# Performance work log

Measured on AMD Instinct MI355X. Metric: run time of the kernel, lower is better.

The kernel has to match this reference:

```python
import jax, jax.numpy as jnp
import numpy as np

LN_EPS = 1e-5
BN_EPS = 1e-5
N_TARGETS = 7


def setup_inputs() -> dict:
    key = jax.random.key(0)
    ks = jax.random.split(key, 12)
    B, N, W, Fin = 64, 40, 256, 64
    H, D = 4, 32
    C = H * D  # gat_out = 128
    L, K = 4, 3  # tcn layers / kernel
    FC = 128
    x = jax.random.normal(ks[0], (B, N, W, Fin), dtype=jnp.float32)
    adj = (jax.random.uniform(ks[1], (N, N)) < 0.3).astype(jnp.float32)
    adj = jnp.maximum(adj, jnp.eye(N, dtype=jnp.float32))  # self-loops
    s = 0.05
    return {
        "x": x,
        "adj": adj,
        "gat_w": jax.random.normal(ks[2], (C, Fin), dtype=jnp.float32) * s,
        "a_src": jax.random.normal(ks[3], (H, D), dtype=jnp.float32) * s,
        "a_dst": jax.random.normal(ks[4], (H, D), dtype=jnp.float32) * s,
        "ln_g": jnp.ones((C,), jnp.float32),
        "ln_b": jnp.zeros((C,), jnp.float32),
        "c1w": jax.random.normal(ks[5], (L, C, C, K), dtype=jnp.float32) * s,
        "c1b": jnp.zeros((L, C), jnp.float32),
        "c2w": jax.random.normal(ks[6], (L, C, C, K), dtype=jnp.float32) * s,
        "c2b": jnp.zeros((L, C), jnp.float32),
        "bn1s": jnp.ones((L, C), jnp.float32),
        "bn1b": jnp.zeros((L, C), jnp.float32),
        "bn1m": jnp.zeros((L, C), jnp.float32),
        "bn1v": jnp.ones((L, C), jnp.float32),
        "bn2s": jnp.ones((L, C), jnp.float32),
        "bn2b": jnp.zeros((L, C), jnp.float32),
        "bn2m": jnp.zeros((L, C), jnp.float32),
        "bn2v": jnp.ones((L, C), jnp.float32),
        "f1w": jax.random.normal(ks[7], (FC, C), dtype=jnp.float32) * s,
        "f1b": jnp.zeros((FC,), jnp.float32),
        "f2w": jax.random.normal(ks[8], (1, FC), dtype=jnp.float32) * s,
        "f2b": jnp.zeros((1,), jnp.float32),
    }


def reference(x, adj, gat_w, a_src, a_dst, ln_g, ln_b,
              c1w, c1b, c2w, c2b,
              bn1s, bn1b, bn1m, bn1v, bn2s, bn2b, bn2m, bn2v,
              f1w, f1b, f2w, f2b):
    B, N, W, Fin = x.shape
    H, D = a_src.shape
    C = H * D
    # --- GAT, vectorized over all W timesteps at once (same math as the per-t loop) ---
    h = jnp.einsum('bnwf,of->bnwo', x, gat_w).reshape(B, N, W, H, D)
    e_src = jnp.einsum('bnwhd,hd->bnwh', h, a_src)  # (B,N,W,H)
    e_dst = jnp.einsum('bnwhd,hd->bnwh', h, a_dst)
    # scores[b,i,w,h,j] = leaky_relu(e_src[b,i] + e_dst[b,j])
    scores = e_src[:, :, :, :, None] + jnp.transpose(e_dst, (0, 2, 3, 1))[:, None]  # (B,N,W,H,N)
    scores = jax.nn.leaky_relu(scores, 0.2)
    mask = adj[None, :, None, None, :] != 0
    scores = jnp.where(mask, scores, -1e9)
    attn = jax.nn.softmax(scores, axis=-1)  # softmax over destination j
    gat = jnp.einsum('bnwhj,bjwhd->bnwhd', attn, h).reshape(B, N, W, C)
    # --- LayerNorm over feature dim ---
    mu = gat.mean(-1, keepdims=True)
    var = gat.var(-1, keepdims=True)
    g = (gat - mu) / jnp.sqrt(var + LN_EPS) * ln_g + ln_b
    # --- TCN over per-node temporal sequences: (B*N, C, W) ---
    seq = jnp.transpose(g.reshape(B * N, W, C), (0, 2, 1))
    K = c1w.shape[-1]

    def bn(z, s, b, m, v):
        return (z - m[None, :, None]) / jnp.sqrt(v[None, :, None] + BN_EPS) * s[None, :, None] + b[None, :, None]

    def cconv(z, w, b, dil):
        pad = (K - 1) * dil  # causal left-padding
        y = jax.lax.conv_general_dilated(z, w, window_strides=(1,), padding=[(pad, 0)],
                                         rhs_dilation=(dil,), dimension_numbers=('NCH', 'OIH', 'NCH'))
        return y + b[None, :, None]

    cur = seq
    for i in range(c1w.shape[0]):  # fixed small number of TCN blocks
        dil = 2 ** i
        o = jax.nn.gelu(bn(cconv(cur, c1w[i], c1b[i], dil), bn1s[i], bn1b[i], bn1m[i], bn1v[i]), approximate=False)
        o = jax.nn.gelu(bn(cconv(o, c2w[i], c2b[i], dil), bn2s[i], bn2b[i], bn2m[i], bn2v[i]), approximate=False)
        cur = jax.nn.gelu(o + cur, approximate=False)  # residual is Identity (in_ch == out_ch)
    h_last = cur[:, :, -1].reshape(B, N, C)
    t = h_last[:, :N_TARGETS, :]  # target_indices = range(7)
    z = jax.nn.gelu(jnp.einsum('bnc,hc->bnh', t, f1w) + f1b, approximate=False)
    logits = (jnp.einsum('bnh,oh->bno', z, f2w) + f2b)[..., 0]  # (B, 7)
    return logits
```

## Files before the change

### kernel.cpp

```cpp
#include <hip/hip_runtime.h>
#include <hip/hip_bf16.h>
#include <math.h>

#define Bb   64
#define Nn   40
#define Ww   256
#define FIN  64
#define Hh   4
#define Dd   32
#define Cc   128
#define NT   7
#define FC   128
#define WT   61
#define W0   195
#define PSTRIDE 520
#define HS2  132

#define GTAUS 2
#define NTG   31
#define XPAN  768
#define GROWS 80

#define SEQHI_OFF  0u
#define SEQ_BYTES  (448u * WT * Cc * 2u)
#define SEQLO_OFF  (SEQHI_OFF + SEQ_BYTES)
#define WBH_OFF    (SEQLO_OFF + SEQ_BYTES)
#define WB_BYTES   (8u * 4u * 24u * 64u * 8u * 2u)
#define WBL_OFF    (WBH_OFF + WB_BYTES)
#define PSB_OFF    (WBL_OFF + WB_BYTES)
#define PSS_OFF    (PSB_OFF + 4096u)
#define PSH_OFF    (PSS_OFF + 4096u)
#define WGH_OFF    (PSH_OFF + 4096u)
#define WGL_OFF    (WGH_OFF + 16384u)
#define WPHASE_US  49152u

typedef __attribute__((ext_vector_type(8)))  short short8;
typedef __attribute__((ext_vector_type(16))) float f32x16;

__device__ __forceinline__ float gelu_exact(float v) {
    const float z = v * 0.70710678118654752440f;
    const float a = fabsf(z);
    const float t = 1.0f / fmaf(0.3275911f, a, 1.0f);
    float p = fmaf(t, 1.061405429f, -1.453152027f);
    p = fmaf(t, p, 1.421413741f);
    p = fmaf(t, p, -0.284496736f);
    p = fmaf(t, p, 0.254829592f);
    p *= t;
    const float e = 1.0f - p * __expf(-a * a);
    const float erfv = copysignf(e, z);
    return 0.5f * v * (1.0f + erfv);
}
__device__ __forceinline__ float b2f(ushort u) {
    union { uint i; float f; } c; c.i = ((uint)u) << 16; return c.f;
}
__device__ __forceinline__ void split_bf16(float v, ushort& h, ushort& l) {
    __hip_bfloat16 bh = __float2bfloat16(v);
    float fh = __bfloat162float(bh);
    __hip_bfloat16 bl = __float2bfloat16(v - fh);
    h = *(ushort*)&bh; l = *(ushort*)&bl;
}

__global__ __launch_bounds__(256) void prep_kernel(
    const float* __restrict__ c1w, const float* __restrict__ c1b,
    const float* __restrict__ c2w, const float* __restrict__ c2b,
    const float* __restrict__ bn1s, const float* __restrict__ bn1b,
    const float* __restrict__ bn1m, const float* __restrict__ bn1v,
    const float* __restrict__ bn2s, const float* __restrict__ bn2b,
    const float* __restrict__ bn2m, const float* __restrict__ bn2v,
    const float* __restrict__ gat_w,
    char* __restrict__ ws)
{
    if (blockIdx.x < 192) {
        const int t = blockIdx.x * 256 + threadIdx.x;
        const int lane  = t & 63;
        const int kstep = (t >> 6) % 24;
        const int nt    = ((t >> 6) / 24) & 3;
        const int p     = (t >> 6) / 96;
        const int l = p >> 1, cv = p & 1;
        const int co = nt * 32 + (lane & 31);
        const float* wsrc = cv ? c2w : c1w;
        ushort* wbh = (ushort*)(ws + WBH_OFF);
        ushort* wbl = (ushort*)(ws + WBL_OFF);
#pragma unroll
        for (int j = 0; j < 8; ++j) {
            const int k  = kstep * 16 + ((lane >> 5) << 3) + j;
            const int kk = k >> 7, ci = k & 127;
            const float w = wsrc[((size_t)(l * Cc + co) * Cc + ci) * 3 + kk];
            ushort h, lo; split_bf16(w, h, lo);
            wbh[(size_t)t * 8 + j] = h;
            wbl[(size_t)t * 8 + j] = lo;
        }
    } else if (blockIdx.x == 192) {
        float* psb = (float*)(ws + PSB_OFF);
        float* pss = (float*)(ws + PSS_OFF);
        float* psh = (float*)(ws + PSH_OFF);
        for (int idx = threadIdx.x; idx < 1024; idx += 256) {
            const int p = idx >> 7, co = idx & 127;
            const int l = p >> 1, cv = p & 1;
            const int lc = l * Cc + co;
            const float s  = cv ? bn2s[lc] : bn1s[lc];
            const float bb = cv ? bn2b[lc] : bn1b[lc];
            const float m  = cv ? bn2m[lc] : bn1m[lc];
            const float vv = cv ? bn2v[lc] : bn1v[lc];
            const float cb = cv ? c2b[lc] : c1b[lc];
            const float scale = s * rsqrtf(vv + 1e-5f);
            pss[idx] = scale;
            psh[idx] = bb - m * scale;
            psb[idx] = cb;
        }
    } else {
        ushort* wgh = (ushort*)(ws + WGH_OFF);
        ushort* wgl = (ushort*)(ws + WGL_OFF);
#pragma unroll
        for (int it = 0; it < 4; ++it) {
            const int t = it * 256 + threadIdx.x;
            const int lane = t & 63;
            const int ks   = (t >> 6) & 3;
            const int nt   = t >> 8;
            const int co   = nt * 32 + (lane & 31);
#pragma unroll
            for (int j = 0; j < 8; ++j) {
                const int k = ks * 16 + ((lane >> 5) << 3) + j;
                ushort h, lo; split_bf16(gat_w[co * FIN + k], h, lo);
                wgh[t * 8 + j] = h;
                wgl[t * 8 + j] = lo;
            }
        }
    }
}

__global__ __launch_bounds__(256) void gat_ln_kernel(
    const float* __restrict__ x, const float* __restrict__ adj,
    const char* __restrict__ ws_ro,
    const float* __restrict__ a_src, const float* __restrict__ a_dst,
    const float* __restrict__ ln_g, const float* __restrict__ ln_b,
    ushort* __restrict__ seq_hi, ushort* __restrict__ seq_lo)
{
    __shared__ __align__(16) char pool[2 * 12288];
    __shared__ __align__(16) float h_lds[GROWS * HS2];

    ushort* xa_hi = (ushort*)pool;
    ushort* xa_lo = (ushort*)(pool + 12288);
    float* e_lds    = (float*)pool;
    float* attn_lds = (float*)(pool + 2560);
    float* g_lds    = (float*)(pool + 11520);

    const int tid = threadIdx.x;
    const int b   = blockIdx.x / NTG;
    const int tg  = blockIdx.x % NTG;
    const int tau0g  = tg * GTAUS;
    const int nvalid = (tau0g + 1 < WT) ? 2 : 1;

    for (int idx = tid; idx < GTAUS * Nn * 8; idx += 256) {
        const int tl  = idx >= 320;
        const int rem = idx - tl * 320;
        const int n  = rem >> 3;
        const int oc = rem & 7;
        if (tl < nvalid) {
            const int w = W0 + tau0g + tl;
            const float* src = x + ((size_t)(b * Nn + n) * Ww + w) * FIN + oc * 8;
            const float4 f0 = *(const float4*)(src);
            const float4 f1 = *(const float4*)(src + 4);
            ushort h[8], l[8];
            split_bf16(f0.x, h[0], l[0]); split_bf16(f0.y, h[1], l[1]);
            split_bf16(f0.z, h[2], l[2]); split_bf16(f0.w, h[3], l[3]);
            split_bf16(f1.x, h[4], l[4]); split_bf16(f1.y, h[5], l[5]);
            split_bf16(f1.z, h[6], l[6]); split_bf16(f1.w, h[7], l[7]);
            const int dst = oc * XPAN + (tl * Nn + n) * 8;
            *(uint4*)(xa_hi + dst) = *(uint4*)h;
            *(uint4*)(xa_lo + dst) = *(uint4*)l;
        }
    }
    __syncthreads();

    {
        const int wave = tid >> 6;
        const int lane = tid & 63;
        const int nt   = wave;
        const int q2   = lane >> 5;
        const int m32  = lane & 31;
        const ushort* WGH = (const ushort*)(ws_ro + WGH_OFF);
        const ushort* WGL = (const ushort*)(ws_ro + WGL_OFF);

        short8 BH[4], BL[4];
#pragma unroll
        for (int ks = 0; ks < 4; ++ks) {
            const size_t wo = ((size_t)((nt * 4 + ks) * 64 + lane)) * 8;
            BH[ks] = *(const short8*)(WGH + wo);
            BL[ks] = *(const short8*)(WGL + wo);
        }
        const int co = nt * 32 + m32;

#pragma unroll
        for (int mt = 0; mt < 3; ++mt) {
            f32x16 acc;
#pragma unroll
            for (int i = 0; i < 16; ++i) acc[i] = 0.f;
#pragma unroll
            for (int ks = 0; ks < 4; ++ks) {
                const int aoff = (ks * 2 + q2) * XPAN + (mt * 32 + m32) * 8;
                const short8 ah = *(const short8*)(xa_hi + aoff);
                const short8 al = *(const short8*)(xa_lo + aoff);
                acc = __builtin_amdgcn_mfma_f32_32x32x16_bf16(ah, BH[ks], acc, 0, 0, 0);
                acc = __builtin_amdgcn_mfma_f32_32x32x16_bf16(al, BH[ks], acc, 0, 0, 0);
                acc = __builtin_amdgcn_mfma_f32_32x32x16_bf16(ah, BL[ks], acc, 0, 0, 0);
            }
#pragma unroll
            for (int reg = 0; reg < 16; ++reg) {
                const int row = mt * 32 + (reg & 3) + 8 * (reg >> 2) + 4 * q2;
                if (row < GROWS) h_lds[row * HS2 + co] = acc[reg];
            }
        }
    }
    __syncthreads();

    for (int u = tid; u < GTAUS * 2 * Nn * Hh; u += 256) {
        const int tl = u >= 320;
        const int uu = u - tl * 320;
        const int s  = uu & 1;
        const int hh = (uu >> 1) & 3;
        const int n  = uu >> 3;
        const float* av = (s ? a_dst : a_src) + hh * Dd;
        const float* hp = h_lds + (tl * Nn + n) * HS2 + hh * Dd;
        float acc = 0.f;
#pragma unroll
        for (int i = 0; i < 8; ++i) {
            const float4 hv = *(const float4*)(hp + i * 4);
            const float4 avv = *(const float4*)(av + i * 4);
            acc += hv.x * avv.x + hv.y * avv.y + hv.z * avv.z + hv.w * avv.w;
        }
        e_lds[((tl * 2 + s) * Nn + n) * Hh + hh] = acc;
    }
    __syncthreads();

    if (tid < GTAUS * NT * Hh) {
        const int tl = tid >= NT * Hh;
        const int i  = tid - tl * NT * Hh;
        const int n  = i >> 2;
        const int hh = i & 3;
        if (tl < nvalid) {
            const float es = e_lds[((tl * 2 + 0) * Nn + n) * Hh + hh];
            float sc[Nn];
            float mx = -1e30f;
#pragma unroll
            for (int j = 0; j < Nn; ++j) {
                float s = es + e_lds[((tl * 2 + 1) * Nn + j) * Hh + hh];
                s = (s > 0.f) ? s : 0.2f * s;
                if (adj[n * Nn + j] == 0.0f) s = -1e9f;
                sc[j] = s;
                mx = fmaxf(mx, s);
            }
            float sum = 0.f;
#pragma unroll
            for (int j = 0; j < Nn; ++j) { const float p = expf(sc[j] - mx); sc[j] = p; sum += p; }
            const float inv = 1.0f / sum;
#pragma unroll
            for (int j = 0; j < Nn; ++j)
                attn_lds[((tl * NT + n) * Hh + hh) * Nn + j] = sc[j] * inv;
        }
    }
    __syncthreads();

    for (int u = tid; u < GTAUS * NT * 32; u += 256) {
        const int tl = u >= NT * 32;
        const int i  = u - tl * NT * 32;
        const int n    = i >> 5;
        const int cq   = i & 31;
        const int c0   = cq * 4;
        const int head = cq >> 3;
        if (tl < nvalid) {
            const float* ap = attn_lds + ((tl * NT + n) * Hh + head) * Nn;
            float4 acc = make_float4(0.f, 0.f, 0.f, 0.f);
            for (int j = 0; j < Nn; ++j) {
                const float a = ap[j];
                const float4 hv = *(const float4*)(h_lds + (tl * Nn + j) * HS2 + c0);
                acc.x += a * hv.x; acc.y += a * hv.y;
                acc.z += a * hv.z; acc.w += a * hv.w;
            }
            *(float4*)(g_lds + (tl * NT + n) * Cc + c0) = acc;
        }
    }
    __syncthreads();

    for (int u = tid; u < GTAUS * NT * 32; u += 256) {
        const int tl = u >= NT * 32;
        const int i  = u - tl * NT * 32;
        const int n  = i >> 5;
        const int lane = u & 31;
        if (tl < nvalid) {
            const float4 v = ((const float4*)(g_lds + (tl * NT + n) * Cc))[lane];
            float s  = v.x + v.y + v.z + v.w;
            float sq = v.x*v.x + v.y*v.y + v.z*v.z + v.w*v.w;
#pragma unroll
            for (int off = 16; off; off >>= 1) {
                s  += __shfl_xor(s, off, 32);
                sq += __shfl_xor(sq, off, 32);
            }
            const float mu   = s * (1.0f / Cc);
            const float rstd = rsqrtf(sq * (1.0f / Cc) - mu * mu + 1e-5f);
            const float4 gg = ((const float4*)ln_g)[lane];
            const float4 bb = ((const float4*)ln_b)[lane];
            float o0 = (v.x - mu) * rstd * gg.x + bb.x;
            float o1 = (v.y - mu) * rstd * gg.y + bb.y;
            float o2 = (v.z - mu) * rstd * gg.z + bb.z;
            float o3 = (v.w - mu) * rstd * gg.w + bb.w;
            const int r = b * NT + n;
            const int tau = tau0g + tl;
            ushort4 uh, ul;
            split_bf16(o0, uh.x, ul.x);
            split_bf16(o1, uh.y, ul.y);
            split_bf16(o2, uh.z, ul.z);
            split_bf16(o3, uh.w, ul.w);
            const int p  = (lane >> 2) * 2 + ((lane >> 1) & 1);
            const int j0 = (lane & 1) * 4;
            const size_t off = ((size_t)(r * 16 + p) * WT + tau) * 8 + j0;
            *(ushort4*)(seq_hi + off) = uh;
            *(ushort4*)(seq_lo + off) = ul;
        }
    }
}

__device__ __forceinline__ void conv_mfma(
    const ushort* in_hi, const ushort* in_lo,
    ushort* out_hi, ushort* out_lo,
    const ushort* __restrict__ wbh, const ushort* __restrict__ wbl,
    const float* __restrict__ psb, const float* __restrict__ pss,
    const float* __restrict__ psh,
    const int tau0, const int d, const int mt, const int nt,
    const int lane, const bool residual)
{
    if (mt * 32 + 31 < tau0) return;

    const int m  = lane & 31;
    const int q2 = lane >> 5;
    const int co = nt * 32 + m;
    const int mbase = mt * 32 + m;

    const float bsv = psb[co], scv = pss[co], shv = psh[co];
    const int colb = ((co >> 4) * 2 + ((co >> 3) & 1)) * PSTRIDE + (co & 7);

    int rA0 = mbase - 2 * d; rA0 = rA0 < 0 ? 0 : rA0;
    int rA1 = mbase - d;     rA1 = rA1 < 0 ? 0 : rA1;
    const int rA2 = mbase;

    const ushort* wb_h = wbh + (size_t)(nt * 24) * 512 + lane * 8;
    const ushort* wb_l = wbl + (size_t)(nt * 24) * 512 + lane * 8;

    f32x16 acc0, acc1;
#pragma unroll
    for (int i = 0; i < 16; ++i) { acc0[i] = 0.f; acc1[i] = 0.f; }

    short8 WH[4], WL[4];
#pragma unroll
    for (int i = 0; i < 4; ++i) {
        WH[i] = *(const short8*)(wb_h + i * 512);
        WL[i] = *(const short8*)(wb_l + i * 512);
    }

#pragma unroll
    for (int ks = 0; ks < 24; ++ks) {
        const int slot = ks & 3;
        const short8 bh = WH[slot];
        const short8 bl = WL[slot];
        if (ks + 4 < 24) {
            WH[slot] = *(const short8*)(wb_h + (ks + 4) * 512);
            WL[slot] = *(const short8*)(wb_l + (ks + 4) * 512);
        }
        const int kk   = ks >> 3;
        const int rowA = (kk == 0) ? rA0 : (kk == 1 ? rA1 : rA2);
        const int aoff = (((ks & 7) << 1) + q2) * PSTRIDE + rowA * 8;
        const short8 ah = *(const short8*)(in_hi + aoff);
        const short8 al = *(const short8*)(in_lo + aoff);
        acc0 = __builtin_amdgcn_mfma_f32_32x32x16_bf16(ah, bh, acc0, 0, 0, 0);
        acc1 = __builtin_amdgcn_mfma_f32_32x32x16_bf16(al, bh, acc1, 0, 0, 0);
        if (ks & 1)
            acc0 = __builtin_amdgcn_mfma_f32_32x32x16_bf16(ah, bl, acc0, 0, 0, 0);
        else
            acc1 = __builtin_amdgcn_mfma_f32_32x32x16_bf16(ah, bl, acc1, 0, 0, 0);
    }
#pragma unroll
    for (int i = 0; i < 16; ++i) acc0[i] += acc1[i];

    float rc[16];
    if (residual) {
#pragma unroll
        for (int reg = 0; reg < 16; ++reg) {
            const int row = (reg & 3) + 8 * (reg >> 2) + 4 * q2;
            const int tau = mt * 32 + row;
            const int off = colb + tau * 8;
            rc[reg] = (tau >= tau0 && tau <= 60)
                    ? (b2f(out_hi[off]) + b2f(out_lo[off])) : 0.f;
        }
    }

#pragma unroll
    for (int reg = 0; reg < 16; ++reg) {
        const int row = (reg & 3) + 8 * (reg >> 2) + 4 * q2;
        const int tau = mt * 32 + row;
        if (tau >= tau0 && tau <= 60) {
            float v = (acc0[reg] + bsv) * scv + shv;
            v = gelu_exact(v);
            if (residual) v = gelu_exact(v + rc[reg]);
            ushort uh, ul; split_bf16(v, uh, ul);
            const int off = colb + tau * 8;
            out_hi[off] = uh; out_lo[off] = ul;
        }
    }
}

__global__ __launch_bounds__(512, 4) void tcn_head_kernel(
    const char* __restrict__ ws,
    const float* __restrict__ f1w, const float* __restrict__ f1b,
    const float* __restrict__ f2w, const float* __restrict__ f2b,
    float* __restrict__ out)
{
    __shared__ __align__(16) ushort cur_hi[16 * PSTRIDE];
    __shared__ __align__(16) ushort cur_lo[16 * PSTRIDE];
    __shared__ __align__(16) ushort o1_hi [16 * PSTRIDE];
    __shared__ __align__(16) ushort o1_lo [16 * PSTRIDE];
    __shared__ float red[FC];

    const int tid = threadIdx.x;
    const int r   = blockIdx.x;

    const ushort* seq_hi = (const ushort*)(ws + SEQHI_OFF);
    const ushort* seq_lo = (const ushort*)(ws + SEQLO_OFF);
    const ushort* WBH    = (const ushort*)(ws + WBH_OFF);
    const ushort* WBL    = (const ushort*)(ws + WBL_OFF);
    const float*  PSB    = (const float*)(ws + PSB_OFF);
    const float*  PSS    = (const float*)(ws + PSS_OFF);
    const float*  PSH    = (const float*)(ws + PSH_OFF);

    {
        const size_t base = (size_t)r * (16 * WT * 8);
        for (int i = tid; i < 16 * WT; i += 512) {
            const int p = i / WT, row = i - p * WT;
            const int dst = p * PSTRIDE + row * 8;
            *(uint4*)(cur_hi + dst) = *(const uint4*)(seq_hi + base + i * 8);
            *(uint4*)(cur_lo + dst) = *(const uint4*)(seq_lo + base + i * 8);
        }
    }
    __syncthreads();

    const int wave = tid >> 6;
    const int lane = tid & 63;
    const int nt   = wave & 3;
    const int mt   = wave >> 2;

    const int tau0_1[4] = {2, 8, 20, 44};
    const int tau0_2[4] = {4, 12, 28, 60};

#pragma unroll
    for (int l = 0; l < 4; ++l) {
        const int d  = 1 << l;
        const int p1 = 2 * l, p2 = 2 * l + 1;
        conv_mfma(cur_hi, cur_lo, o1_hi, o1_lo,
                  WBH + (size_t)p1 * WPHASE_US, WBL + (size_t)p1 * WPHASE_US,
                  PSB + p1 * Cc, PSS + p1 * Cc, PSH + p1 * Cc,
                  tau0_1[l], d, mt, nt, lane, false);
        __syncthreads();
        conv_mfma(o1_hi, o1_lo, cur_hi, cur_lo,
                  WBH + (size_t)p2 * WPHASE_US, WBL + (size_t)p2 * WPHASE_US,
                  PSB + p2 * Cc, PSS + p2 * Cc, PSH + p2 * Cc,
                  tau0_2[l], d, mt, nt, lane, true);
        __syncthreads();
    }

    if (tid < FC) {
        const float4* wr = (const float4*)(f1w + tid * Cc);
        float acc = 0.f;
#pragma unroll
        for (int i = 0; i < Cc / 4; ++i) {
            const float4 wv = wr[i];
            const int ci0 = i * 4;
            const int off = ((ci0 >> 4) * 2 + ((ci0 >> 3) & 1)) * PSTRIDE
                          + 60 * 8 + (ci0 & 7);
            const ushort4 vh = *(const ushort4*)(cur_hi + off);
            const ushort4 vl = *(const ushort4*)(cur_lo + off);
            acc += wv.x * (b2f(vh.x) + b2f(vl.x))
                 + wv.y * (b2f(vh.y) + b2f(vl.y))
                 + wv.z * (b2f(vh.z) + b2f(vl.z))
                 + wv.w * (b2f(vh.w) + b2f(vl.w));
        }
        red[tid] = gelu_exact(acc + f1b[tid]) * f2w[tid];
    }
    __syncthreads();
    if (tid < 64) {
        float v = red[tid] + red[tid + 64];
#pragma unroll
        for (int off = 32; off; off >>= 1) v += __shfl_xor(v, off, 64);
        if (tid == 0) out[r] = v + f2b[0];
    }
}

extern "C" void kernel_launch(void* const* d_in, const int* in_sizes, int n_in,
                              void* d_out, int out_size, void* d_ws, size_t ws_size,
                              hipStream_t stream) {
    const float* x     = (const float*)d_in[0];
    const float* adj   = (const float*)d_in[1];
    const float* gat_w = (const float*)d_in[2];
    const float* a_src = (const float*)d_in[3];
    const float* a_dst = (const float*)d_in[4];
    const float* ln_g  = (const float*)d_in[5];
    const float* ln_b  = (const float*)d_in[6];
    const float* c1w   = (const float*)d_in[7];
    const float* c1b   = (const float*)d_in[8];
    const float* c2w   = (const float*)d_in[9];
    const float* c2b   = (const float*)d_in[10];
    const float* bn1s  = (const float*)d_in[11];
    const float* bn1b  = (const float*)d_in[12];
    const float* bn1m  = (const float*)d_in[13];
    const float* bn1v  = (const float*)d_in[14];
    const float* bn2s  = (const float*)d_in[15];
    const float* bn2b  = (const float*)d_in[16];
    const float* bn2m  = (const float*)d_in[17];
    const float* bn2v  = (const float*)d_in[18];
    const float* f1w   = (const float*)d_in[19];
    const float* f1b   = (const float*)d_in[20];
    const float* f2w   = (const float*)d_in[21];
    const float* f2b   = (const float*)d_in[22];

    char* ws = (char*)d_ws;

    prep_kernel<<<194, 256, 0, stream>>>(c1w, c1b, c2w, c2b,
        bn1s, bn1b, bn1m, bn1v, bn2s, bn2b, bn2m, bn2v, gat_w, ws);

    gat_ln_kernel<<<Bb * NTG, 256, 0, stream>>>(
        x, adj, ws, a_src, a_dst, ln_g, ln_b,
        (ushort*)(ws + SEQHI_OFF), (ushort*)(ws + SEQLO_OFF));

    tcn_head_kernel<<<Bb * NT, 512, 0, stream>>>(
        ws, f1w, f1b, f2w, f2b, (float*)d_out);
}
```

Measured before the change: 376.5 us.

## Fuse prep into GAT kernel and split TCN conv K-dimension across waves

Merges the weight-prep launch into the GAT kernel as extra leading blocks, and each GAT block now splits gat_w to bf16 hi/lo itself instead of reading a prepped copy. The TCN conv changes from splitting time rows across the two wave groups to splitting the K reduction. Each wave group computes partial sums for both 32-row tiles over half of K, then the halves are combined through LDS scratch that reuses the o1 buffer. This keeps both wave groups busy when the first row tile is fully masked by causal padding. It costs one fewer launch but adds extra syncs and a scratch round-trip per conv.

Measured after the change: 364.6 us (median of 2 runs). 3.2% less time.

```diff
diff --git a/kernel.cpp b/kernel.cpp
--- a/kernel.cpp
+++ b/kernel.cpp
@@ -20,6 +20,7 @@
 #define NTG   31
 #define XPAN  768
 #define GROWS 80
+#define PREPB 193
 
 #define SEQHI_OFF  0u
 #define SEQ_BYTES  (448u * WT * Cc * 2u)
@@ -30,8 +31,6 @@
 #define PSB_OFF    (WBL_OFF + WB_BYTES)
 #define PSS_OFF    (PSB_OFF + 4096u)
 #define PSH_OFF    (PSS_OFF + 4096u)
-#define WGH_OFF    (PSH_OFF + 4096u)
-#define WGL_OFF    (WGH_OFF + 16384u)
 #define WPHASE_US  49152u
 
 typedef __attribute__((ext_vector_type(8)))  short short8;
@@ -60,84 +59,67 @@
     h = *(ushort*)&bh; l = *(ushort*)&bl;
 }
 
-__global__ __launch_bounds__(256) void prep_kernel(
+__global__ __launch_bounds__(256) void gat_prep_kernel(
+    const float* __restrict__ x, const float* __restrict__ adj,
+    const float* __restrict__ gat_w,
+    const float* __restrict__ a_src, const float* __restrict__ a_dst,
+    const float* __restrict__ ln_g, const float* __restrict__ ln_b,
     const float* __restrict__ c1w, const float* __restrict__ c1b,
     const float* __restrict__ c2w, const float* __restrict__ c2b,
     const float* __restrict__ bn1s, const float* __restrict__ bn1b,
     const float* __restrict__ bn1m, const float* __restrict__ bn1v,
     const float* __restrict__ bn2s, const float* __restrict__ bn2b,
     const float* __restrict__ bn2m, const float* __restrict__ bn2v,
-    const float* __restrict__ gat_w,
-    char* __restrict__ ws)
-{
-    if (blockIdx.x < 192) {
-        const int t = blockIdx.x * 256 + threadIdx.x;
-        const int lane  = t & 63;
-        const int kstep = (t >> 6) % 24;
-        const int nt    = ((t >> 6) / 24) & 3;
-        const int p     = (t >> 6) / 96;
-        const int l = p >> 1, cv = p & 1;
-        const int co = nt * 32 + (lane & 31);
-        const float* wsrc = cv ? c2w : c1w;
-        ushort* wbh = (ushort*)(ws + WBH_OFF);
-        ushort* wbl = (ushort*)(ws + WBL_OFF);
-#pragma unroll
-        for (int j = 0; j < 8; ++j) {
-            const int k  = kstep * 16 + ((lane >> 5) << 3) + j;
-            const int kk = k >> 7, ci = k & 127;
-            const float w = wsrc[((size_t)(l * Cc + co) * Cc + ci) * 3 + kk];
-            ushort h, lo; split_bf16(w, h, lo);
-            wbh[(size_t)t * 8 + j] = h;
-            wbl[(size_t)t * 8 + j] = lo;
-        }
-    } else if (blockIdx.x == 192) {
-        float* psb = (float*)(ws + PSB_OFF);
-        float* pss = (float*)(ws + PSS_OFF);
-        float* psh = (float*)(ws + PSH_OFF);
-        for (int idx = threadIdx.x; idx < 1024; idx += 256) {
-            const int p = idx >> 7, co = idx & 127;
-            const int l = p >> 1, cv = p & 1;
-            const int lc = l * Cc + co;
-            const float s  = cv ? bn2s[lc] : bn1s[lc];
-            const float bb = cv ? bn2b[lc] : bn1b[lc];
-            const float m  = cv ? bn2m[lc] : bn1m[lc];
-            const float vv = cv ? bn2v[lc] : bn1v[lc];
-            const float cb = cv ? c2b[lc] : c1b[lc];
-            const float scale = s * rsqrtf(vv + 1e-5f);
-            pss[idx] = scale;
-            psh[idx] = bb - m * scale;
-            psb[idx] = cb;
-        }
-    } else {
-        ushort* wgh = (ushort*)(ws + WGH_OFF);
-        ushort* wgl = (ushort*)(ws + WGL_OFF);
-#pragma unroll
-        for (int it = 0; it < 4; ++it) {
-            const int t = it * 256 + threadIdx.x;
-            const int lane = t & 63;
-            const int ks   = (t >> 6) & 3;
-            const int nt   = t >> 8;
-            const int co   = nt * 32 + (lane & 31);
-#pragma unroll
-            for (int j = 0; j < 8; ++j) {
-                const int k = ks * 16 + ((lane >> 5) << 3) + j;
-                ushort h, lo; split_bf16(gat_w[co * FIN + k], h, lo);
-                wgh[t * 8 + j] = h;
-                wgl[t * 8 + j] = lo;
-            }
-        }
-    }
-}
-
-__global__ __launch_bounds__(256) void gat_ln_kernel(
-    const float* __restrict__ x, const float* __restrict__ adj,
-    const char* __restrict__ ws_ro,
-    const float* __restrict__ a_src, const float* __restrict__ a_dst,
-    const float* __restrict__ ln_g, const float* __restrict__ ln_b,
+    char* __restrict__ ws,
     ushort* __restrict__ seq_hi, ushort* __restrict__ seq_lo)
 {
     __shared__ __align__(16) char pool[2 * 12288];
     __shared__ __align__(16) float h_lds[GROWS * HS2];
+
+    const int tid = threadIdx.x;
+
+    if (blockIdx.x < PREPB) {
+        if (blockIdx.x < 192) {
+            const int t = blockIdx.x * 256 + tid;
+            const int lane  = t & 63;
+            const int kstep = (t >> 6) % 24;
+            const int nt    = ((t >> 6) / 24) & 3;
+            const int p     = (t >> 6) / 96;
+            const int l = p >> 1, cv = p & 1;
+            const int co = nt * 32 + (lane & 31);
+            const float* wsrc = cv ? c2w : c1w;
+            ushort* wbh = (ushort*)(ws + WBH_OFF);
+            ushort* wbl = (ushort*)(ws + WBL_OFF);
+#pragma unroll
+            for (int j = 0; j < 8; ++j) {
+                const int k  = kstep * 16 + ((lane >> 5) << 3) + j;
+                const int kk = k >> 7, ci = k & 127;
+                const float w = wsrc[((size_t)(l * Cc + co) * Cc + ci) * 3 + kk];
+                ushort h, lo; split_bf16(w, h, lo);
+                wbh[(size_t)t * 8 + j] = h;
+                wbl[(size_t)t * 8 + j] = lo;
+            }
+        } else {
+            float* psb = (float*)(ws + PSB_OFF);
+            float* pss = (float*)(ws + PSS_OFF);
+            float* psh = (float*)(ws + PSH_OFF);
+            for (int idx = tid; idx < 1024; idx += 256) {
+                const int p = idx >> 7, co = idx & 127;
+                const int l = p >> 1, cv = p & 1;
+                const int lc = l * Cc + co;
+                const float s  = cv ? bn2s[lc] : bn1s[lc];
+                const float bb = cv ? bn2b[lc] : bn1b[lc];
+                const float m  = cv ? bn2m[lc] : bn1m[lc];
+                const float vv = cv ? bn2v[lc] : bn1v[lc];
+                const float cb = cv ? c2b[lc] : c1b[lc];
+                const float scale = s * rsqrtf(vv + 1e-5f);
+                pss[idx] = scale;
+                psh[idx] = bb - m * scale;
+                psb[idx] = cb;
+            }
+        }
+        return;
+    }
 
     ushort* xa_hi = (ushort*)pool;
     ushort* xa_lo = (ushort*)(pool + 12288);
@@ -145,9 +127,9 @@
     float* attn_lds = (float*)(pool + 2560);
     float* g_lds    = (float*)(pool + 11520);
 
-    const int tid = threadIdx.x;
-    const int b   = blockIdx.x / NTG;
-    const int tg  = blockIdx.x % NTG;
+    const int blk = blockIdx.x - PREPB;
+    const int b   = blk / NTG;
+    const int tg  = blk % NTG;
     const int tau0g  = tg * GTAUS;
     const int nvalid = (tau0g + 1 < WT) ? 2 : 1;
 
@@ -179,17 +161,22 @@
         const int nt   = wave;
         const int q2   = lane >> 5;
         const int m32  = lane & 31;
-        const ushort* WGH = (const ushort*)(ws_ro + WGH_OFF);
-        const ushort* WGL = (const ushort*)(ws_ro + WGL_OFF);
+        const int co   = nt * 32 + m32;
 
         short8 BH[4], BL[4];
 #pragma unroll
         for (int ks = 0; ks < 4; ++ks) {
-            const size_t wo = ((size_t)((nt * 4 + ks) * 64 + lane)) * 8;
-            BH[ks] = *(const short8*)(WGH + wo);
-            BL[ks] = *(const short8*)(WGL + wo);
-        }
-        const int co = nt * 32 + m32;
+            const float* gp = gat_w + co * FIN + ks * 16 + q2 * 8;
+            const float4 f0 = *(const float4*)(gp);
+            const float4 f1 = *(const float4*)(gp + 4);
+            ushort h[8], l[8];
+            split_bf16(f0.x, h[0], l[0]); split_bf16(f0.y, h[1], l[1]);
+            split_bf16(f0.z, h[2], l[2]); split_bf16(f0.w, h[3], l[3]);
+            split_bf16(f1.x, h[4], l[4]); split_bf16(f1.y, h[5], l[5]);
+            split_bf16(f1.z, h[6], l[6]); split_bf16(f1.w, h[7], l[7]);
+            BH[ks] = *(short8*)h;
+            BL[ks] = *(short8*)l;
+        }
 
 #pragma unroll
         for (int mt = 0; mt < 3; ++mt) {
@@ -320,90 +307,120 @@
     }
 }
 
-__device__ __forceinline__ void conv_mfma(
+__device__ __forceinline__ void conv_sk(
     const ushort* in_hi, const ushort* in_lo,
     ushort* out_hi, ushort* out_lo,
+    float* scratch,
     const ushort* __restrict__ wbh, const ushort* __restrict__ wbl,
     const float* __restrict__ psb, const float* __restrict__ pss,
     const float* __restrict__ psh,
-    const int tau0, const int d, const int mt, const int nt,
+    const int tau0, const int d, const int kh, const int nt,
     const int lane, const bool residual)
 {
-    if (mt * 32 + 31 < tau0) return;
-
     const int m  = lane & 31;
     const int q2 = lane >> 5;
+    const bool skipA = (tau0 > 31);
+
+    int rA0a = m - 2 * d; rA0a = rA0a < 0 ? 0 : rA0a;
+    int rA1a = m - d;     rA1a = rA1a < 0 ? 0 : rA1a;
+    const int rA2a = m;
+    const int rA0b = 32 + m - 2 * d;
+    const int rA1b = 32 + m - d;
+    const int rA2b = 32 + m;
+
+    const ushort* wb_h = wbh + (size_t)(nt * 24 + kh * 12) * 512 + lane * 8;
+    const ushort* wb_l = wbl + (size_t)(nt * 24 + kh * 12) * 512 + lane * 8;
+
     const int co = nt * 32 + m;
-    const int mbase = mt * 32 + m;
-
     const float bsv = psb[co], scv = pss[co], shv = psh[co];
     const int colb = ((co >> 4) * 2 + ((co >> 3) & 1)) * PSTRIDE + (co & 7);
 
-    int rA0 = mbase - 2 * d; rA0 = rA0 < 0 ? 0 : rA0;
-    int rA1 = mbase - d;     rA1 = rA1 < 0 ? 0 : rA1;
-    const int rA2 = mbase;
-
-    const ushort* wb_h = wbh + (size_t)(nt * 24) * 512 + lane * 8;
-    const ushort* wb_l = wbl + (size_t)(nt * 24) * 512 + lane * 8;
-
-    f32x16 acc0, acc1;
-#pragma unroll
-    for (int i = 0; i < 16; ++i) { acc0[i] = 0.f; acc1[i] = 0.f; }
-
-    short8 WH[4], WL[4];
-#pragma unroll
-    for (int i = 0; i < 4; ++i) {
+    f32x16 accA, accB;
+#pragma unroll
+    for (int i = 0; i < 16; ++i) { accA[i] = 0.f; accB[i] = 0.f; }
+
+    short8 WH[3], WL[3];
+#pragma unroll
+    for (int i = 0; i < 3; ++i) {
         WH[i] = *(const short8*)(wb_h + i * 512);
         WL[i] = *(const short8*)(wb_l + i * 512);
     }
 
 #pragma unroll
-    for (int ks = 0; ks < 24; ++ks) {
-        const int slot = ks & 3;
+    for (int i = 0; i < 12; ++i) {
+        const int slot = i % 3;
         const short8 bh = WH[slot];
         const short8 bl = WL[slot];
-        if (ks + 4 < 24) {
-            WH[slot] = *(const short8*)(wb_h + (ks + 4) * 512);
-            WL[slot] = *(const short8*)(wb_l + (ks + 4) * 512);
-        }
-        const int kk   = ks >> 3;
-        const int rowA = (kk == 0) ? rA0 : (kk == 1 ? rA1 : rA2);
-        const int aoff = (((ks & 7) << 1) + q2) * PSTRIDE + rowA * 8;
-        const short8 ah = *(const short8*)(in_hi + aoff);
-        const short8 al = *(const short8*)(in_lo + aoff);
-        acc0 = __builtin_amdgcn_mfma_f32_32x32x16_bf16(ah, bh, acc0, 0, 0, 0);
-        acc1 = __builtin_amdgcn_mfma_f32_32x32x16_bf16(al, bh, acc1, 0, 0, 0);
-        if (ks & 1)
-            acc0 = __builtin_amdgcn_mfma_f32_32x32x16_bf16(ah, bl, acc0, 0, 0, 0);
-        else
-            acc1 = __builtin_amdgcn_mfma_f32_32x32x16_bf16(ah, bl, acc1, 0, 0, 0);
-    }
-#pragma unroll
-    for (int i = 0; i < 16; ++i) acc0[i] += acc1[i];
-
-    float rc[16];
-    if (residual) {
+        if (i + 3 < 12) {
+            WH[slot] = *(const short8*)(wb_h + (i + 3) * 512);
+            WL[slot] = *(const short8*)(wb_l + (i + 3) * 512);
+        }
+        const int ks = kh * 12 + i;
+        const int kk = ks >> 3;
+        const int panel = (((ks & 7) << 1) + q2) * PSTRIDE;
+        if (!skipA) {
+            const int ra = (kk == 0) ? rA0a : (kk == 1 ? rA1a : rA2a);
+            const short8 ahA = *(const short8*)(in_hi + panel + ra * 8);
+            const short8 alA = *(const short8*)(in_lo + panel + ra * 8);
+            accA = __builtin_amdgcn_mfma_f32_32x32x16_bf16(ahA, bh, accA, 0, 0, 0);
+            accA = __builtin_amdgcn_mfma_f32_32x32x16_bf16(alA, bh, accA, 0, 0, 0);
+            accA = __builtin_amdgcn_mfma_f32_32x32x16_bf16(ahA, bl, accA, 0, 0, 0);
+        }
+        {
+            const int rb = (kk == 0) ? rA0b : (kk == 1 ? rA1b : rA2b);
+            const short8 ahB = *(const short8*)(in_hi + panel + rb * 8);
+            const short8 alB = *(const short8*)(in_lo + panel + rb * 8);
+            accB = __builtin_amdgcn_mfma_f32_32x32x16_bf16(ahB, bh, accB, 0, 0, 0);
+            accB = __builtin_amdgcn_mfma_f32_32x32x16_bf16(alB, bh, accB, 0, 0, 0);
+            accB = __builtin_amdgcn_mfma_f32_32x32x16_bf16(ahB, bl, accB, 0, 0, 0);
+        }
+    }
+
+    if (residual) __syncthreads();
+
+    if (kh == 0) {
+        float* dst = scratch + ((4 + nt) << 10) + lane;
+#pragma unroll
+        for (int r = 0; r < 16; ++r) dst[r * 64] = accB[r];
+    } else if (!skipA) {
+        float* dst = scratch + (nt << 10) + lane;
+#pragma unroll
+        for (int r = 0; r < 16; ++r) dst[r * 64] = accA[r];
+    }
+    __syncthreads();
+
+    f32x16 acc;
+    if (kh == 0) {
+        acc = accA;
+        if (!skipA) {
+            const float* srcp = scratch + (nt << 10) + lane;
+#pragma unroll
+            for (int r = 0; r < 16; ++r) acc[r] += srcp[r * 64];
+        }
+    } else {
+        acc = accB;
+        const float* srcp = scratch + ((4 + nt) << 10) + lane;
+#pragma unroll
+        for (int r = 0; r < 16; ++r) acc[r] += srcp[r * 64];
+    }
+
+    if (!residual) __syncthreads();
+
+    if (!(skipA && kh == 0)) {
+        const int mt = kh;
 #pragma unroll
         for (int reg = 0; reg < 16; ++reg) {
             const int row = (reg & 3) + 8 * (reg >> 2) + 4 * q2;
             const int tau = mt * 32 + row;
-            const int off = colb + tau * 8;
-            rc[reg] = (tau >= tau0 && tau <= 60)
-                    ? (b2f(out_hi[off]) + b2f(out_lo[off])) : 0.f;
-        }
-    }
-
-#pragma unroll
-    for (int reg = 0; reg < 16; ++reg) {
-        const int row = (reg & 3) + 8 * (reg >> 2) + 4 * q2;
-        const int tau = mt * 32 + row;
-        if (tau >= tau0 && tau <= 60) {
-            float v = (acc0[reg] + bsv) * scv + shv;
-            v = gelu_exact(v);
-            if (residual) v = gelu_exact(v + rc[reg]);
-            ushort uh, ul; split_bf16(v, uh, ul);
-            const int off = colb + tau * 8;
-            out_hi[off] = uh; out_lo[off] = ul;
+            if (tau >= tau0 && tau <= 60) {
+                float v = (acc[reg] + bsv) * scv + shv;
+                v = gelu_exact(v);
+                const int off = colb + tau * 8;
+                if (residual)
+                    v = gelu_exact(v + b2f(out_hi[off]) + b2f(out_lo[off]));
+                ushort uh, ul; split_bf16(v, uh, ul);
+                out_hi[off] = uh; out_lo[off] = ul;
+            }
         }
     }
 }
@@ -416,9 +433,12 @@
 {
     __shared__ __align__(16) ushort cur_hi[16 * PSTRIDE];
     __shared__ __align__(16) ushort cur_lo[16 * PSTRIDE];
-    __shared__ __align__(16) ushort o1_hi [16 * PSTRIDE];
-    __shared__ __align__(16) ushort o1_lo [16 * PSTRIDE];
+    __shared__ __align__(16) ushort o1_pair[2][16 * PSTRIDE];
     __shared__ float red[FC];
+
+    ushort* o1_hi = o1_pair[0];
+    ushort* o1_lo = o1_pair[1];
+    float*  scratch = (float*)o1_pair;
 
     const int tid = threadIdx.x;
     const int r   = blockIdx.x;
@@ -445,7 +465,7 @@
     const int wave = tid >> 6;
     const int lane = tid & 63;
     const int nt   = wave & 3;
-    const int mt   = wave >> 2;
+    const int kh   = wave >> 2;
 
     const int tau0_1[4] = {2, 8, 20, 44};
     const int tau0_2[4] = {4, 12, 28, 60};
@@ -454,15 +474,15 @@
     for (int l = 0; l < 4; ++l) {
         const int d  = 1 << l;
         const int p1 = 2 * l, p2 = 2 * l + 1;
-        conv_mfma(cur_hi, cur_lo, o1_hi, o1_lo,
-                  WBH + (size_t)p1 * WPHASE_US, WBL + (size_t)p1 * WPHASE_US,
-                  PSB + p1 * Cc, PSS + p1 * Cc, PSH + p1 * Cc,
-                  tau0_1[l], d, mt, nt, lane, false);
+        conv_sk(cur_hi, cur_lo, o1_hi, o1_lo, scratch,
+                WBH + (size_t)p1 * WPHASE_US, WBL + (size_t)p1 * WPHASE_US,
+                PSB + p1 * Cc, PSS + p1 * Cc, PSH + p1 * Cc,
+                tau0_1[l], d, kh, nt, lane, false);
         __syncthreads();
-        conv_mfma(o1_hi, o1_lo, cur_hi, cur_lo,
-                  WBH + (size_t)p2 * WPHASE_US, WBL + (size_t)p2 * WPHASE_US,
-                  PSB + p2 * Cc, PSS + p2 * Cc, PSH + p2 * Cc,
-                  tau0_2[l], d, mt, nt, lane, true);
+        conv_sk(o1_hi, o1_lo, cur_hi, cur_lo, scratch,
+                WBH + (size_t)p2 * WPHASE_US, WBL + (size_t)p2 * WPHASE_US,
+                PSB + p2 * Cc, PSS + p2 * Cc, PSH + p2 * Cc,
+                tau0_2[l], d, kh, nt, lane, true);
         __syncthreads();
     }
 
@@ -522,12 +542,11 @@
 
     char* ws = (char*)d_ws;
 
-    prep_kernel<<<194, 256, 0, stream>>>(c1w, c1b, c2w, c2b,
-        bn1s, bn1b, bn1m, bn1v, bn2s, bn2b, bn2m, bn2v, gat_w, ws);
-
-    gat_ln_kernel<<<Bb * NTG, 256, 0, stream>>>(
-        x, adj, ws, a_src, a_dst, ln_g, ln_b,
-        (ushort*)(ws + SEQHI_OFF), (ushort*)(ws + SEQLO_OFF));
+    gat_prep_kernel<<<PREPB + Bb * NTG, 256, 0, stream>>>(
+        x, adj, gat_w, a_src, a_dst, ln_g, ln_b,
+        c1w, c1b, c2w, c2b,
+        bn1s, bn1b, bn1m, bn1v, bn2s, bn2b, bn2m, bn2v,
+        ws, (ushort*)(ws + SEQHI_OFF), (ushort*)(ws + SEQLO_OFF));
 
     tcn_head_kernel<<<Bb * NT, 512, 0, stream>>>(
         ws, f1w, f1b, f2w, f2b, (float*)d_out);
```
